# Optimization experiments

Measured on AMD Instinct MI355X. Metric: run time of the kernel, lower is better.

The kernel has to match this reference:

```python
import jax, jax.numpy as jnp
import numpy as np

B, INPUT_DIM, EMB_DIM = 16384, 2048, 768
DOMAIN_NUM, MEMORY_NUM, TAU = 9, 10, 32.0


def setup_inputs() -> dict:
    key = jax.random.key(0)
    k1, k2, k3, k4, k5 = jax.random.split(key, 5)
    feature = jax.random.normal(k1, (B, INPUT_DIM), dtype=jnp.float32)
    category = jax.random.randint(k2, (B,), 0, DOMAIN_NUM, dtype=jnp.int64)
    # Linear(input_dim, emb_dim, bias=False) weights: [emb_dim, input_dim]
    W_topic = jax.random.normal(k3, (EMB_DIM, INPUT_DIM), dtype=jnp.float32) * 0.02
    W_domain = jax.random.normal(k4, (EMB_DIM, INPUT_DIM), dtype=jnp.float32) * 0.02
    # domain_num Embedding(memory_num, emb_dim) tables, stacked: [D, M, E]
    memory_tables = jax.random.normal(k5, (DOMAIN_NUM, MEMORY_NUM, EMB_DIM), dtype=jnp.float32)
    return {"feature": feature, "W_topic": W_topic, "W_domain": W_domain,
            "memory_tables": memory_tables, "category": category}


def reference(feature, W_topic, W_domain, memory_tables, category):
    eps = 1e-12
    # F.normalize(feature, p=2, dim=-1)
    norm = jnp.maximum(jnp.linalg.norm(feature, axis=-1, keepdims=True), eps)
    feat = feature / norm                                   # [B, I]
    # per-sample gather of each sample's category memory table: [B, M, E]
    mem = memory_tables[category]
    # faithful quirk: loop over domain_num indexes the BATCH dim of the stack
    D = memory_tables.shape[0]
    mems_d = mem[:D]                                        # [D, M, E]
    t = feat @ W_topic.T                                    # [B, E]
    topic_att = jax.nn.softmax(jnp.einsum('be,dme->bdm', t, mems_d) * TAU, axis=-1)
    sep = jnp.einsum('bdm,dme->bde', topic_att, mems_d)     # [B, D, E]
    dproj = feat @ W_domain.T                               # [B, E]
    domain_att = jax.nn.softmax(jnp.einsum('bde,be->bd', sep, dproj) * TAU, axis=-1)
    return domain_att[:, None, :]                           # [B, 1, D]
```

## Files before the change

### kernel.cpp

```cpp
#include <hip/hip_runtime.h>
#include <math.h>

#define TAU_F 32.0f

typedef __attribute__((ext_vector_type(8))) _Float16 half8;
typedef __attribute__((ext_vector_type(2))) __fp16 half2v;
typedef __attribute__((ext_vector_type(4))) float f32x4;

union HU { uint4 u; half8 v; };

__device__ __forceinline__ void sync_lds_only() {
    asm volatile("s_waitcnt lgkmcnt(0)" ::: "memory");
    __builtin_amdgcn_s_barrier();
}

__global__ __launch_bounds__(256) void gproj2(
    const float* __restrict__ Wt, const float* __restrict__ Wd,
    const float* __restrict__ mem, const int* __restrict__ cat,
    float* __restrict__ P)
{
    __shared__ float Ml[96 * 36];
    __shared__ float Wl[32 * 68];

    const int bid = blockIdx.x;
    const int mat = bid >> 7;
    const int ks  = (bid >> 5) & 3;
    const int ct  = bid & 31;
    const int c0  = ct * 64;
    const int tid = threadIdx.x;
    const float* __restrict__ W = mat ? Wd : Wt;

    const int tr = tid >> 4;
    const int tc = tid & 15;

    float acc[6][4];
    #pragma unroll
    for (int j = 0; j < 6; ++j)
        #pragma unroll
        for (int q = 0; q < 4; ++q) acc[j][q] = 0.f;

    for (int ch = 0; ch < 6; ++ch) {
        __syncthreads();
        #pragma unroll
        for (int p = 0; p < 3; ++p) {
            const int idx = tid + 256 * p;
            const int r   = idx >> 3;
            const int kq  = idx & 7;
            float4 v = make_float4(0.f, 0.f, 0.f, 0.f);
            if (r < 90) {
                const int d = r / 10;
                const int mrow = cat[d] * 10 + (r - d * 10);
                v = *(const float4*)(mem + (size_t)mrow * 768 + ks * 192 + ch * 32 + kq * 4);
            }
            *(float4*)(Ml + r * 36 + kq * 4) = v;
        }
        #pragma unroll
        for (int p = 0; p < 2; ++p) {
            const int idx = tid + 256 * p;
            const int e   = idx >> 4;
            const int c4  = (idx & 15) * 4;
            *(float4*)(Wl + e * 68 + c4) =
                *(const float4*)(W + (size_t)(ks * 192 + ch * 32 + e) * 2048 + c0 + c4);
        }
        __syncthreads();

        #pragma unroll
        for (int e = 0; e < 32; e += 4) {
            float4 m4[6], w4[4];
            #pragma unroll
            for (int j = 0; j < 6; ++j) m4[j] = *(const float4*)(Ml + (tr * 6 + j) * 36 + e);
            #pragma unroll
            for (int q = 0; q < 4; ++q) w4[q] = *(const float4*)(Wl + (e + q) * 68 + tc * 4);
            #pragma unroll
            for (int j = 0; j < 6; ++j) {
                const float mv[4] = {m4[j].x, m4[j].y, m4[j].z, m4[j].w};
                #pragma unroll
                for (int q = 0; q < 4; ++q) {
                    acc[j][0] = fmaf(mv[q], w4[q].x, acc[j][0]);
                    acc[j][1] = fmaf(mv[q], w4[q].y, acc[j][1]);
                    acc[j][2] = fmaf(mv[q], w4[q].z, acc[j][2]);
                    acc[j][3] = fmaf(mv[q], w4[q].w, acc[j][3]);
                }
            }
        }
    }

    #pragma unroll
    for (int j = 0; j < 6; ++j) {
        float4 v = make_float4(acc[j][0], acc[j][1], acc[j][2], acc[j][3]);
        *(float4*)(P + (size_t)ks * 393216 + (size_t)(mat * 96 + tr * 6 + j) * 2048 + c0 + tc * 4) = v;
    }
}

__global__ __launch_bounds__(256) void split_g3(
    const float* __restrict__ P, unsigned short* __restrict__ gB)
{
    const int u  = blockIdx.x * 256 + threadIdx.x;
    const int n  = u >> 8;
    const int k0 = (u & 255) * 8;

    float s[8] = {0.f, 0.f, 0.f, 0.f, 0.f, 0.f, 0.f, 0.f};
    #pragma unroll
    for (int ks = 0; ks < 4; ++ks) {
        const float4 a = *(const float4*)(P + (size_t)ks * 393216 + (size_t)n * 2048 + k0);
        const float4 b = *(const float4*)(P + (size_t)ks * 393216 + (size_t)n * 2048 + k0 + 4);
        s[0] += a.x; s[1] += a.y; s[2] += a.z; s[3] += a.w;
        s[4] += b.x; s[5] += b.y; s[6] += b.z; s[7] += b.w;
    }
    union { _Float16 h[8]; uint4 u4; } hi, lo;
    #pragma unroll
    for (int e = 0; e < 8; ++e) {
        const _Float16 h = (_Float16)s[e];
        hi.h[e] = h;
        lo.h[e] = (_Float16)(s[e] - (float)h);
    }
    const int kc = k0 >> 5;
    const int lq = (k0 >> 3) & 3;
    const int nq = n / 48;
    const int rm = n - nq * 48;
    const int j  = rm >> 4;
    const int lm = rm & 15;
    const size_t fH = (size_t)((kc * 12 + nq * 3 + j) * 2 + 0) * 512 + lq * 128 + lm * 8;
    const size_t fL = (size_t)((kc * 12 + nq * 3 + j) * 2 + 1) * 512 + lq * 128 + lm * 8;
    *(uint4*)(gB + fH) = hi.u4;
    *(uint4*)(gB + fL) = lo.u4;
}

__global__ __launch_bounds__(256, 2) void fused_mfma6(
    const float* __restrict__ feat, const unsigned short* __restrict__ gB,
    float* __restrict__ P2, float* __restrict__ ssqp)
{
    __shared__ __align__(16) unsigned short aS[4 * 64 * 44];

    const int tid = threadIdx.x;
    const int rt  = blockIdx.x >> 1;
    const int ks  = blockIdx.x & 1;
    const int row0 = rt * 64;

    const int w  = tid >> 6, l = tid & 63;
    const int lm = l & 15,  lq = l >> 4;
    const int nq = (w + blockIdx.x) & 3;
    const bool topic = (nq < 2);
    const int r8 = tid >> 2, kq = tid & 3;

    f32x4 acc[4][3];
    #pragma unroll
    for (int i = 0; i < 4; ++i)
        #pragma unroll
        for (int j = 0; j < 3; ++j) acc[i][j] = (f32x4)0.f;
    float ssq = 0.f;

    const float* fbase = feat + (size_t)(row0 + r8) * 2048 + ks * 1024 + kq * 8;
    const unsigned short* bbase = gB + (size_t)ks * 393216 + nq * 3072 + l * 8;

    float4 c0a = *(const float4*)(fbase);
    float4 c0b = *(const float4*)(fbase + 4);
    float4 c1a = *(const float4*)(fbase + 32);
    float4 c1b = *(const float4*)(fbase + 36);
    uint4 bh[3], bl[3];
    #pragma unroll
    for (int j = 0; j < 3; ++j) bh[j] = *(const uint4*)(bbase + j * 1024);
    if (topic) {
        #pragma unroll
        for (int j = 0; j < 3; ++j) bl[j] = *(const uint4*)(bbase + j * 1024 + 512);
    }

    auto cw = [&](int buf, float4 va, float4 vb) {
        const float xs[8] = {va.x, va.y, va.z, va.w, vb.x, vb.y, vb.z, vb.w};
        union { half2v h2[4]; uint4 u4; } uh, ul;
        #pragma unroll
        for (int e = 0; e < 4; ++e) {
            const float a = xs[2 * e], b = xs[2 * e + 1];
            ssq = fmaf(a, a, ssq); ssq = fmaf(b, b, ssq);
            half2v h = __builtin_amdgcn_cvt_pkrtz(a, b);
            uh.h2[e] = h;
            ul.h2[e] = __builtin_amdgcn_cvt_pkrtz(a - (float)h[0], b - (float)h[1]);
        }
        *(uint4*)(aS + (size_t)((buf * 2 + 0) * 64 + r8) * 44 + kq * 8) = uh.u4;
        *(uint4*)(aS + (size_t)((buf * 2 + 1) * 64 + r8) * 44 + kq * 8) = ul.u4;
    };

    cw(0, c0a, c0b);
    sync_lds_only();

    for (int kc = 0; kc < 32; ++kc) {
        const int kb = (kc + 1 < 32) ? kc + 1 : 31;
        uint4 bhn[3], bln[3];
        #pragma unroll
        for (int j = 0; j < 3; ++j)
            bhn[j] = *(const uint4*)(bbase + (size_t)kb * 12288 + j * 1024);
        if (topic) {
            #pragma unroll
            for (int j = 0; j < 3; ++j)
                bln[j] = *(const uint4*)(bbase + (size_t)kb * 12288 + j * 1024 + 512);
        }
        const int ka = (kc + 2 < 32) ? kc + 2 : 31;
        float4 cna = *(const float4*)(fbase + ka * 32);
        float4 cnb = *(const float4*)(fbase + ka * 32 + 4);

        if (kc < 31) cw((kc + 1) & 1, c1a, c1b);

        const int cb = kc & 1;
        half8 fh[4], fl[4];
        #pragma unroll
        for (int i = 0; i < 4; ++i) {
            HU th;
            th.u = *(const uint4*)(aS + (size_t)((cb * 2 + 0) * 64 + i * 16 + lm) * 44 + lq * 8);
            fh[i] = th.v;
        }
        if (topic) {
            #pragma unroll
            for (int i = 0; i < 4; ++i) {
                HU tl;
                tl.u = *(const uint4*)(aS + (size_t)((cb * 2 + 1) * 64 + i * 16 + lm) * 44 + lq * 8);
                fl[i] = tl.v;
            }
        }

        if (topic) {
            #pragma unroll
            for (int j = 0; j < 3; ++j) {
                HU h8, l8; h8.u = bh[j]; l8.u = bl[j];
                #pragma unroll
                for (int i = 0; i < 4; ++i) {
                    acc[i][j] = __builtin_amdgcn_mfma_f32_16x16x32_f16(fh[i], h8.v, acc[i][j], 0, 0, 0);
                    acc[i][j] = __builtin_amdgcn_mfma_f32_16x16x32_f16(fh[i], l8.v, acc[i][j], 0, 0, 0);
                    acc[i][j] = __builtin_amdgcn_mfma_f32_16x16x32_f16(fl[i], h8.v, acc[i][j], 0, 0, 0);
                }
            }
        } else {
            #pragma unroll
            for (int j = 0; j < 3; ++j) {
                HU h8; h8.u = bh[j];
                #pragma unroll
                for (int i = 0; i < 4; ++i)
                    acc[i][j] = __builtin_amdgcn_mfma_f32_16x16x32_f16(fh[i], h8.v, acc[i][j], 0, 0, 0);
            }
        }

        sync_lds_only();

        c1a = cna; c1b = cnb;
        #pragma unroll
        for (int j = 0; j < 3; ++j) bh[j] = bhn[j];
        if (topic) {
            #pragma unroll
            for (int j = 0; j < 3; ++j) bl[j] = bln[j];
        }
    }

    ssq += __shfl_xor(ssq, 1, 64);
    ssq += __shfl_xor(ssq, 2, 64);
    if (kq == 0) ssqp[(size_t)ks * 16384 + row0 + r8] = ssq;

    #pragma unroll
    for (int i = 0; i < 4; ++i)
        #pragma unroll
        for (int j = 0; j < 3; ++j)
            #pragma unroll
            for (int r = 0; r < 4; ++r)
                P2[((size_t)ks * 16384 + row0 + i * 16 + lq * 4 + r) * 192 + nq * 48 + j * 16 + lm]
                    = acc[i][j][r];
}

#define EP_SPAD 196
__global__ __launch_bounds__(256) void ep_kernel(
    const float* __restrict__ P2, const float* __restrict__ ssqp,
    float* __restrict__ out)
{
    __shared__ float sc[64 * EP_SPAD];
    const int tid  = threadIdx.x;
    const int row0 = blockIdx.x * 64;

    float4 s[12];
    #pragma unroll
    for (int p = 0; p < 12; ++p) s[p] = make_float4(0.f, 0.f, 0.f, 0.f);
    #pragma unroll
    for (int ks = 0; ks < 2; ++ks)
        #pragma unroll
        for (int p = 0; p < 12; ++p) {
            const int u   = p * 256 + tid;
            const int row = u / 48;
            const int c4  = (u - row * 48) * 4;
            const float4 v = *(const float4*)(P2 + ((size_t)ks * 16384 + row0 + row) * 192 + c4);
            s[p].x += v.x; s[p].y += v.y; s[p].z += v.z; s[p].w += v.w;
        }
    #pragma unroll
    for (int p = 0; p < 12; ++p) {
        const int u   = p * 256 + tid;
        const int row = u / 48;
        const int c4  = (u - row * 48) * 4;
        *(float4*)(sc + row * EP_SPAD + c4) = s[p];
    }
    float nsq = 0.f;
    if (tid < 64) {
        nsq = ssqp[row0 + tid] + ssqp[16384 + row0 + tid];
    }
    __syncthreads();

    if (tid < 64) {
        const int r = tid;
        const float inv = TAU_F / fmaxf(sqrtf(nsq), 1e-12f);
        const float* scr = sc + (size_t)r * EP_SPAD;
        float lg[9];
        float dmax = -1e30f;
        #pragma unroll
        for (int d = 0; d < 9; ++d) {
            const float* v = scr + d * 10;
            const float* u = scr + 96 + d * 10;
            float mx = v[0];
            #pragma unroll
            for (int m = 1; m < 10; ++m) mx = fmaxf(mx, v[m]);
            float ssum = 0.f, dot = 0.f;
            #pragma unroll
            for (int m = 0; m < 10; ++m) {
                const float p = __expf((v[m] - mx) * inv);
                ssum += p;
                dot = fmaf(p, u[m], dot);
            }
            const float lgt = (dot / ssum) * inv;
            lg[d] = lgt;
            dmax = fmaxf(dmax, lgt);
        }
        float s2 = 0.f;
        #pragma unroll
        for (int d = 0; d < 9; ++d) { const float p = __expf(lg[d] - dmax); lg[d] = p; s2 += p; }
        const float r2 = 1.0f / s2;
        #pragma unroll
        for (int d = 0; d < 9; ++d)
            out[(size_t)(row0 + r) * 9 + d] = lg[d] * r2;
    }
}

extern "C" void kernel_launch(void* const* d_in, const int* in_sizes, int n_in,
                              void* d_out, int out_size, void* d_ws, size_t ws_size,
                              hipStream_t stream) {
    const float* feature = (const float*)d_in[0];
    const float* Wt      = (const float*)d_in[1];
    const float* Wd      = (const float*)d_in[2];
    const float* mem     = (const float*)d_in[3];
    const int*   cat     = (const int*)d_in[4];

    float* P2 = (float*)d_ws;
    float* P  = (float*)d_ws;
    unsigned short* gB = (unsigned short*)((char*)d_ws + 50331648);
    float* ssqp = (float*)((char*)d_ws + 50331648 + 1572864);
    float* out = (float*)d_out;

    gproj2<<<256, 256, 0, stream>>>(Wt, Wd, mem, cat, P);
    split_g3<<<192, 256, 0, stream>>>(P, gB);
    fused_mfma6<<<512, 256, 0, stream>>>(feature, gB, P2, ssqp);
    ep_kernel<<<256, 256, 0, stream>>>(P2, ssqp, out);
}
```

Before: 251.9 us.

## Fuse epilogue into MFMA GEMM, dropping split-K for 32-row tiles

Removes the split-K decomposition and the separate epilogue kernel. Each block now covers 32 rows across the full K=2048, runs two K sub-chunks per iteration, writes its accumulators to shared memory and computes the two-level softmax in place, with pairs of threads splitting the domains. This avoids writing and re-reading the partial-sum buffer (about 25MB) and one kernel launch. In exchange the weight operand is reloaded for twice as many row tiles, and the per-block M tile is smaller, so MFMA reuse of B fragments drops.

```diff
diff --git a/kernel.cpp b/kernel.cpp
--- a/kernel.cpp
+++ b/kernel.cpp
@@ -126,44 +126,34 @@
     *(uint4*)(gB + fL) = lo.u4;
 }
 
-__global__ __launch_bounds__(256, 2) void fused_mfma6(
+__global__ __launch_bounds__(256, 2) void fused_ep(
     const float* __restrict__ feat, const unsigned short* __restrict__ gB,
-    float* __restrict__ P2, float* __restrict__ ssqp)
+    float* __restrict__ out)
 {
-    __shared__ __align__(16) unsigned short aS[4 * 64 * 44];
-
-    const int tid = threadIdx.x;
-    const int rt  = blockIdx.x >> 1;
-    const int ks  = blockIdx.x & 1;
-    const int row0 = rt * 64;
+    __shared__ __align__(16) unsigned char smraw[32 * 193 * 4];
+    unsigned short* aS = (unsigned short*)smraw;
+    float* sc = (float*)smraw;
+    __shared__ float ssqS[32];
+
+    const int tid  = threadIdx.x;
+    const int row0 = blockIdx.x * 32;
 
     const int w  = tid >> 6, l = tid & 63;
     const int lm = l & 15,  lq = l >> 4;
     const int nq = (w + blockIdx.x) & 3;
     const bool topic = (nq < 2);
-    const int r8 = tid >> 2, kq = tid & 3;
-
-    f32x4 acc[4][3];
-    #pragma unroll
-    for (int i = 0; i < 4; ++i)
+    const int sr = tid >> 3, kq = tid & 7;
+    const int skf = kq >> 2, sk4 = kq & 3;
+
+    f32x4 acc[2][3];
+    #pragma unroll
+    for (int i = 0; i < 2; ++i)
         #pragma unroll
         for (int j = 0; j < 3; ++j) acc[i][j] = (f32x4)0.f;
     float ssq = 0.f;
 
-    const float* fbase = feat + (size_t)(row0 + r8) * 2048 + ks * 1024 + kq * 8;
-    const unsigned short* bbase = gB + (size_t)ks * 393216 + nq * 3072 + l * 8;
-
-    float4 c0a = *(const float4*)(fbase);
-    float4 c0b = *(const float4*)(fbase + 4);
-    float4 c1a = *(const float4*)(fbase + 32);
-    float4 c1b = *(const float4*)(fbase + 36);
-    uint4 bh[3], bl[3];
-    #pragma unroll
-    for (int j = 0; j < 3; ++j) bh[j] = *(const uint4*)(bbase + j * 1024);
-    if (topic) {
-        #pragma unroll
-        for (int j = 0; j < 3; ++j) bl[j] = *(const uint4*)(bbase + j * 1024 + 512);
-    }
+    const float* fbase = feat + (size_t)(row0 + sr) * 2048 + kq * 8;
+    const unsigned short* bbase = gB + nq * 3072 + l * 8;
 
     auto cw = [&](int buf, float4 va, float4 vb) {
         const float xs[8] = {va.x, va.y, va.z, va.w, vb.x, vb.y, vb.z, vb.w};
@@ -176,159 +166,146 @@
             uh.h2[e] = h;
             ul.h2[e] = __builtin_amdgcn_cvt_pkrtz(a - (float)h[0], b - (float)h[1]);
         }
-        *(uint4*)(aS + (size_t)((buf * 2 + 0) * 64 + r8) * 44 + kq * 8) = uh.u4;
-        *(uint4*)(aS + (size_t)((buf * 2 + 1) * 64 + r8) * 44 + kq * 8) = ul.u4;
+        *(uint4*)(aS + (size_t)(((buf * 2 + 0) * 2 + skf) * 32 + sr) * 40 + sk4 * 8) = uh.u4;
+        *(uint4*)(aS + (size_t)(((buf * 2 + 1) * 2 + skf) * 32 + sr) * 40 + sk4 * 8) = ul.u4;
     };
 
+    float4 c0a = *(const float4*)(fbase);
+    float4 c0b = *(const float4*)(fbase + 4);
+    float4 c1a = *(const float4*)(fbase + 64);
+    float4 c1b = *(const float4*)(fbase + 68);
     cw(0, c0a, c0b);
     sync_lds_only();
 
-    for (int kc = 0; kc < 32; ++kc) {
-        const int kb = (kc + 1 < 32) ? kc + 1 : 31;
-        uint4 bhn[3], bln[3];
+    for (int kt = 0; kt < 32; ++kt) {
+        uint4 bh[6], bl[6];
+        #pragma unroll
+        for (int kf = 0; kf < 2; ++kf)
+            #pragma unroll
+            for (int j = 0; j < 3; ++j)
+                bh[kf * 3 + j] = *(const uint4*)(bbase + (size_t)(2 * kt + kf) * 12288 + j * 1024);
+        if (topic) {
+            #pragma unroll
+            for (int kf = 0; kf < 2; ++kf)
+                #pragma unroll
+                for (int j = 0; j < 3; ++j)
+                    bl[kf * 3 + j] = *(const uint4*)(bbase + (size_t)(2 * kt + kf) * 12288 + j * 1024 + 512);
+        }
+        const int ka = (kt + 2 < 32) ? kt + 2 : 31;
+        float4 cna = *(const float4*)(fbase + ka * 64);
+        float4 cnb = *(const float4*)(fbase + ka * 64 + 4);
+
+        if (kt < 31) cw((kt + 1) & 1, c1a, c1b);
+
+        const int cb = kt & 1;
+        half8 fh[2][2], fl[2][2];
+        #pragma unroll
+        for (int i = 0; i < 2; ++i)
+            #pragma unroll
+            for (int kf = 0; kf < 2; ++kf) {
+                HU t;
+                t.u = *(const uint4*)(aS + (size_t)(((cb * 2 + 0) * 2 + kf) * 32 + i * 16 + lm) * 40 + lq * 8);
+                fh[i][kf] = t.v;
+            }
+        if (topic) {
+            #pragma unroll
+            for (int i = 0; i < 2; ++i)
+                #pragma unroll
+                for (int kf = 0; kf < 2; ++kf) {
+                    HU t;
+                    t.u = *(const uint4*)(aS + (size_t)(((cb * 2 + 1) * 2 + kf) * 32 + i * 16 + lm) * 40 + lq * 8);
+                    fl[i][kf] = t.v;
+                }
+        }
+
+        if (topic) {
+            #pragma unroll
+            for (int j = 0; j < 3; ++j)
+                #pragma unroll
+                for (int kf = 0; kf < 2; ++kf) {
+                    HU h8, l8; h8.u = bh[kf * 3 + j]; l8.u = bl[kf * 3 + j];
+                    #pragma unroll
+                    for (int i = 0; i < 2; ++i) {
+                        acc[i][j] = __builtin_amdgcn_mfma_f32_16x16x32_f16(fh[i][kf], h8.v, acc[i][j], 0, 0, 0);
+                        acc[i][j] = __builtin_amdgcn_mfma_f32_16x16x32_f16(fh[i][kf], l8.v, acc[i][j], 0, 0, 0);
+                        acc[i][j] = __builtin_amdgcn_mfma_f32_16x16x32_f16(fl[i][kf], h8.v, acc[i][j], 0, 0, 0);
+                    }
+                }
+        } else {
+            #pragma unroll
+            for (int j = 0; j < 3; ++j)
+                #pragma unroll
+                for (int kf = 0; kf < 2; ++kf) {
+                    HU h8; h8.u = bh[kf * 3 + j];
+                    #pragma unroll
+                    for (int i = 0; i < 2; ++i)
+                        acc[i][j] = __builtin_amdgcn_mfma_f32_16x16x32_f16(fh[i][kf], h8.v, acc[i][j], 0, 0, 0);
+                }
+        }
+
+        sync_lds_only();
+        c1a = cna; c1b = cnb;
+    }
+
+    #pragma unroll
+    for (int i = 0; i < 2; ++i)
         #pragma unroll
         for (int j = 0; j < 3; ++j)
-            bhn[j] = *(const uint4*)(bbase + (size_t)kb * 12288 + j * 1024);
-        if (topic) {
-            #pragma unroll
-            for (int j = 0; j < 3; ++j)
-                bln[j] = *(const uint4*)(bbase + (size_t)kb * 12288 + j * 1024 + 512);
-        }
-        const int ka = (kc + 2 < 32) ? kc + 2 : 31;
-        float4 cna = *(const float4*)(fbase + ka * 32);
-        float4 cnb = *(const float4*)(fbase + ka * 32 + 4);
-
-        if (kc < 31) cw((kc + 1) & 1, c1a, c1b);
-
-        const int cb = kc & 1;
-        half8 fh[4], fl[4];
-        #pragma unroll
-        for (int i = 0; i < 4; ++i) {
-            HU th;
-            th.u = *(const uint4*)(aS + (size_t)((cb * 2 + 0) * 64 + i * 16 + lm) * 44 + lq * 8);
-            fh[i] = th.v;
-        }
-        if (topic) {
-            #pragma unroll
-            for (int i = 0; i < 4; ++i) {
-                HU tl;
-                tl.u = *(const uint4*)(aS + (size_t)((cb * 2 + 1) * 64 + i * 16 + lm) * 44 + lq * 8);
-                fl[i] = tl.v;
-            }
-        }
-
-        if (topic) {
-            #pragma unroll
-            for (int j = 0; j < 3; ++j) {
-                HU h8, l8; h8.u = bh[j]; l8.u = bl[j];
-                #pragma unroll
-                for (int i = 0; i < 4; ++i) {
-                    acc[i][j] = __builtin_amdgcn_mfma_f32_16x16x32_f16(fh[i], h8.v, acc[i][j], 0, 0, 0);
-                    acc[i][j] = __builtin_amdgcn_mfma_f32_16x16x32_f16(fh[i], l8.v, acc[i][j], 0, 0, 0);
-                    acc[i][j] = __builtin_amdgcn_mfma_f32_16x16x32_f16(fl[i], h8.v, acc[i][j], 0, 0, 0);
-                }
-            }
-        } else {
-            #pragma unroll
-            for (int j = 0; j < 3; ++j) {
-                HU h8; h8.u = bh[j];
-                #pragma unroll
-                for (int i = 0; i < 4; ++i)
-                    acc[i][j] = __builtin_amdgcn_mfma_f32_16x16x32_f16(fh[i], h8.v, acc[i][j], 0, 0, 0);
-            }
-        }
-
-        sync_lds_only();
-
-        c1a = cna; c1b = cnb;
-        #pragma unroll
-        for (int j = 0; j < 3; ++j) bh[j] = bhn[j];
-        if (topic) {
-            #pragma unroll
-            for (int j = 0; j < 3; ++j) bl[j] = bln[j];
-        }
-    }
+            #pragma unroll
+            for (int r4 = 0; r4 < 4; ++r4)
+                sc[(i * 16 + lq * 4 + r4) * 193 + nq * 48 + j * 16 + lm] = acc[i][j][r4];
 
     ssq += __shfl_xor(ssq, 1, 64);
     ssq += __shfl_xor(ssq, 2, 64);
-    if (kq == 0) ssqp[(size_t)ks * 16384 + row0 + r8] = ssq;
-
-    #pragma unroll
-    for (int i = 0; i < 4; ++i)
-        #pragma unroll
-        for (int j = 0; j < 3; ++j)
-            #pragma unroll
-            for (int r = 0; r < 4; ++r)
-                P2[((size_t)ks * 16384 + row0 + i * 16 + lq * 4 + r) * 192 + nq * 48 + j * 16 + lm]
-                    = acc[i][j][r];
-}
-
-#define EP_SPAD 196
-__global__ __launch_bounds__(256) void ep_kernel(
-    const float* __restrict__ P2, const float* __restrict__ ssqp,
-    float* __restrict__ out)
-{
-    __shared__ float sc[64 * EP_SPAD];
-    const int tid  = threadIdx.x;
-    const int row0 = blockIdx.x * 64;
-
-    float4 s[12];
-    #pragma unroll
-    for (int p = 0; p < 12; ++p) s[p] = make_float4(0.f, 0.f, 0.f, 0.f);
-    #pragma unroll
-    for (int ks = 0; ks < 2; ++ks)
-        #pragma unroll
-        for (int p = 0; p < 12; ++p) {
-            const int u   = p * 256 + tid;
-            const int row = u / 48;
-            const int c4  = (u - row * 48) * 4;
-            const float4 v = *(const float4*)(P2 + ((size_t)ks * 16384 + row0 + row) * 192 + c4);
-            s[p].x += v.x; s[p].y += v.y; s[p].z += v.z; s[p].w += v.w;
-        }
-    #pragma unroll
-    for (int p = 0; p < 12; ++p) {
-        const int u   = p * 256 + tid;
-        const int row = u / 48;
-        const int c4  = (u - row * 48) * 4;
-        *(float4*)(sc + row * EP_SPAD + c4) = s[p];
-    }
-    float nsq = 0.f;
+    ssq += __shfl_xor(ssq, 4, 64);
+    if (kq == 0) ssqS[sr] = ssq;
+    __syncthreads();
+
     if (tid < 64) {
-        nsq = ssqp[row0 + tid] + ssqp[16384 + row0 + tid];
-    }
-    __syncthreads();
-
-    if (tid < 64) {
-        const int r = tid;
-        const float inv = TAU_F / fmaxf(sqrtf(nsq), 1e-12f);
-        const float* scr = sc + (size_t)r * EP_SPAD;
-        float lg[9];
+        const int r  = tid >> 1, hf = tid & 1;
+        const int nd = hf ? 4 : 5;
+        const int d0 = hf ? 5 : 0;
+        const float inv = TAU_F / fmaxf(sqrtf(ssqS[r]), 1e-12f);
+        const float* scr = sc + (size_t)r * 193;
+        float lg[5];
         float dmax = -1e30f;
         #pragma unroll
-        for (int d = 0; d < 9; ++d) {
-            const float* v = scr + d * 10;
-            const float* u = scr + 96 + d * 10;
-            float mx = v[0];
-            #pragma unroll
-            for (int m = 1; m < 10; ++m) mx = fmaxf(mx, v[m]);
-            float ssum = 0.f, dot = 0.f;
-            #pragma unroll
-            for (int m = 0; m < 10; ++m) {
-                const float p = __expf((v[m] - mx) * inv);
-                ssum += p;
-                dot = fmaf(p, u[m], dot);
+        for (int dd = 0; dd < 5; ++dd) {
+            if (dd < nd) {
+                const int d = d0 + dd;
+                const float* v = scr + d * 10;
+                const float* u = scr + 96 + d * 10;
+                float mx = v[0];
+                #pragma unroll
+                for (int m = 1; m < 10; ++m) mx = fmaxf(mx, v[m]);
+                float ssum = 0.f, dot = 0.f;
+                #pragma unroll
+                for (int m = 0; m < 10; ++m) {
+                    const float p = __expf((v[m] - mx) * inv);
+                    ssum += p;
+                    dot = fmaf(p, u[m], dot);
+                }
+                const float lgt = (dot / ssum) * inv;
+                lg[dd] = lgt;
+                dmax = fmaxf(dmax, lgt);
+            } else {
+                lg[dd] = -1e30f;
             }
-            const float lgt = (dot / ssum) * inv;
-            lg[d] = lgt;
-            dmax = fmaxf(dmax, lgt);
-        }
+        }
+        dmax = fmaxf(dmax, __shfl_xor(dmax, 1, 64));
         float s2 = 0.f;
         #pragma unroll
-        for (int d = 0; d < 9; ++d) { const float p = __expf(lg[d] - dmax); lg[d] = p; s2 += p; }
+        for (int dd = 0; dd < 5; ++dd) {
+            const float p = __expf(lg[dd] - dmax);
+            lg[dd] = p;
+            s2 += p;
+        }
+        s2 += __shfl_xor(s2, 1, 64);
         const float r2 = 1.0f / s2;
         #pragma unroll
-        for (int d = 0; d < 9; ++d)
-            out[(size_t)(row0 + r) * 9 + d] = lg[d] * r2;
+        for (int dd = 0; dd < 5; ++dd)
+            if (dd < nd)
+                out[(size_t)(row0 + r) * 9 + d0 + dd] = lg[dd] * r2;
     }
 }
 
@@ -341,14 +318,11 @@
     const float* mem     = (const float*)d_in[3];
     const int*   cat     = (const int*)d_in[4];
 
-    float* P2 = (float*)d_ws;
     float* P  = (float*)d_ws;
     unsigned short* gB = (unsigned short*)((char*)d_ws + 50331648);
-    float* ssqp = (float*)((char*)d_ws + 50331648 + 1572864);
     float* out = (float*)d_out;
 
     gproj2<<<256, 256, 0, stream>>>(Wt, Wd, mem, cat, P);
     split_g3<<<192, 256, 0, stream>>>(P, gB);
-    fused_mfma6<<<512, 256, 0, stream>>>(feature, gB, P2, ssqp);
-    ep_kernel<<<256, 256, 0, stream>>>(P2, ssqp, out);
-}
+    fused_ep<<<512, 256, 0, stream>>>(feature, gB, out);
+}
```

New measurement: 243.0 us. 3.6% less time.
